# Kernel optimization log

Measured on AMD Instinct MI355X. Metric: run time of the kernel, lower is better.

The kernel has to match this reference:

```python
import jax, jax.numpy as jnp
import numpy as np

N = 100000
E = 1600000
U_DIM = 8
H_DIM = 64
MLP_H = 32
LRELU_SLOPE = 0.01  # torch LeakyReLU default


def _linear_params(key, fan_in, fan_out):
    # torch nn.Linear init: U(-1/sqrt(fan_in), 1/sqrt(fan_in))
    k1, k2 = jax.random.split(key)
    bound = 1.0 / np.sqrt(fan_in)
    W = jax.random.uniform(k1, (fan_in, fan_out), minval=-bound, maxval=bound, dtype=jnp.float32)
    b = jax.random.uniform(k2, (fan_out,), minval=-bound, maxval=bound, dtype=jnp.float32)
    return W, b


def setup_inputs() -> dict:
    key = jax.random.key(0)
    ks = jax.random.split(key, 9)
    h = jax.random.normal(ks[0], (N, H_DIM), dtype=jnp.float32)
    u = jax.random.normal(ks[1], (N, U_DIM), dtype=jnp.float32)
    pos = jax.random.normal(ks[2], (N, 2), dtype=jnp.float32)
    src = jax.random.randint(ks[3], (E,), 0, N)
    dst = jax.random.randint(ks[4], (E,), 0, N)
    # edge MLP (u2h_enc): in = 4 + u_dim + h_dim
    W1e, b1e = _linear_params(ks[5], 4 + U_DIM + H_DIM, MLP_H)
    W2e, b2e = _linear_params(ks[6], MLP_H, H_DIM)
    # node MLP (h_updater): in = 2 + 2*h_dim + u_dim
    W1n, b1n = _linear_params(ks[7], 2 + 2 * H_DIM + U_DIM, MLP_H)
    W2n, b2n = _linear_params(ks[8], MLP_H, H_DIM)
    return {"h": h, "u": u, "pos": pos, "src": src, "dst": dst,
            "W1e": W1e, "b1e": b1e, "W2e": W2e, "b2e": b2e,
            "W1n": W1n, "b1n": b1n, "W2n": W2n, "b2n": b2n}


def _mlp(x, W1, b1, W2, b2):
    # Linear -> LeakyReLU -> Linear -> Tanh
    y = x @ W1 + b1
    y = jnp.where(y >= 0, y, LRELU_SLOPE * y)
    return jnp.tanh(y @ W2 + b2)


def reference(h, u, pos, src, dst, W1e, b1e, W2e, b2e, W1n, b1n, W2n, b2n):
    # gather: edge message input [E, 4+u+h]
    edge_inp = jnp.concatenate([pos[src], pos[dst], u[src], h[src]], axis=-1)
    msg = _mlp(edge_inp, W1e, b1e, W2e, b2e)  # [E, h_dim]
    # scatter-sum into destination nodes
    sum_h = jax.ops.segment_sum(msg, dst, num_segments=N)  # [N, h_dim]
    node_inp = jnp.concatenate([pos, h, sum_h, u], axis=-1)  # [N, 2+2h+u]
    return _mlp(node_inp, W1n, b1n, W2n, b2n)
```

## Files before the change

kernel.cpp:

```cpp
#include <hip/hip_runtime.h>


#define LRELU_SLOPE 0.01f
#define BUCK_SHIFT 8
#define TANH_SCALE 2.8853900817779268f

constexpr int OFF_B1E   = 2432;
constexpr int OFF_B2E   = 4512;
constexpr int OFF_B2N   = 11104;
constexpr int OFF_B1N   = 11168;
constexpr int OFF_W1POS = 11200;
constexpr int W_TOTAL   = 11264;

typedef __bf16 bf16x8 __attribute__((ext_vector_type(8)));
typedef float  f32x4  __attribute__((ext_vector_type(4)));

__device__ __forceinline__ unsigned f2bf_pair(float f0, float f1) {
    unsigned u0 = __float_as_uint(f0), u1 = __float_as_uint(f1);
    unsigned r0 = (u0 + 0x7fffu + ((u0 >> 16) & 1u)) >> 16;
    unsigned r1 = (u1 + 0x7fffu + ((u1 >> 16) & 1u)) >> 16;
    return r0 | (r1 << 16);
}
__device__ __forceinline__ float bf_lo(unsigned p) { return __uint_as_float(p << 16); }
__device__ __forceinline__ float bf_hi(unsigned p) { return __uint_as_float(p & 0xffff0000u); }
__device__ __forceinline__ float bf_round(float f) {
    unsigned u = __float_as_uint(f);
    return __uint_as_float((u + 0x7fffu + ((u >> 16) & 1u)) & 0xffff0000u);
}
__device__ __forceinline__ bf16x8 pack8(float a0, float a1, float a2, float a3,
                                        float a4, float a5, float a6, float a7) {
    union { uint4 u; bf16x8 b; } c;
    c.u.x = f2bf_pair(a0, a1); c.u.y = f2bf_pair(a2, a3);
    c.u.z = f2bf_pair(a4, a5); c.u.w = f2bf_pair(a6, a7);
    return c.b;
}

__device__ __forceinline__ float w1e_x96(const float* W1e, int i, int j) {
    if (i < 64) return W1e[(12 + i) * 32 + j];
    if (i == 64) return W1e[0 * 32 + j];
    if (i == 65) return W1e[1 * 32 + j];
    if (i >= 68 && i < 76) return W1e[(4 + i - 68) * 32 + j];
    return 0.f;
}
__device__ __forceinline__ float w1n_x96(const float* W1n, int i, int j) {
    if (i < 64) return W1n[(2 + i) * 32 + j];
    if (i == 64) return W1n[0 * 32 + j];
    if (i == 65) return W1n[1 * 32 + j];
    if (i >= 68 && i < 76) return W1n[(130 + i - 68) * 32 + j];
    return 0.f;
}

__global__ void prep_weights(const float* __restrict__ W1e, const float* __restrict__ b1e,
                             const float* __restrict__ W2e, const float* __restrict__ b2e,
                             const float* __restrict__ W1n, const float* __restrict__ b1n,
                             const float* __restrict__ W2n, const float* __restrict__ b2n,
                             float* __restrict__ Wf, uint4* __restrict__ fragW2,
                             uint4* __restrict__ frag1, uint4* __restrict__ frag2,
                             uint4* __restrict__ fragE, uint4* __restrict__ fragN,
                             int* __restrict__ gcnt, int nbuck) {
    int t = blockIdx.x * blockDim.x + threadIdx.x;
    int T = gridDim.x * blockDim.x;
    for (int idx = t; idx < nbuck; idx += T) gcnt[idx] = 0;
    for (int idx = t; idx < 32; idx += T)   Wf[OFF_B1E + idx] = b1e[idx];
    for (int idx = t; idx < 64; idx += T)   Wf[OFF_B2E + idx] = b2e[idx] * TANH_SCALE;
    for (int idx = t; idx < 64; idx += T)   Wf[OFF_B2N + idx] = b2n[idx];
    for (int idx = t; idx < 32; idx += T)   Wf[OFF_B1N + idx] = b1n[idx];
    for (int idx = t; idx < 32; idx += T) {
        Wf[OFF_W1POS + 2 * idx + 0] = W1e[2 * 32 + idx];
        Wf[OFF_W1POS + 2 * idx + 1] = W1e[3 * 32 + idx];
    }
    for (int idx = t; idx < 256; idx += T) {
        int tt = idx >> 6, l = idx & 63;
        int colv = l & 15, quadv = l >> 4;
        uint4 v;
        unsigned pk[4];
#pragma unroll
        for (int pr = 0; pr < 4; pr++) {
            int j0 = quadv * 8 + 2 * pr;
            float f0 = W2e[j0 * 64 + 16 * tt + colv] * TANH_SCALE;
            float f1 = W2e[(j0 + 1) * 64 + 16 * tt + colv] * TANH_SCALE;
            pk[pr] = f2bf_pair(f0, f1);
        }
        v.x = pk[0]; v.y = pk[1]; v.z = pk[2]; v.w = pk[3];
        fragW2[tt * 64 + l] = v;
    }
    for (int idx = t; idx < 512; idx += T) {
        int l = idx & 63, rest = idx >> 6;
        int hl = rest & 1, tt = (rest >> 1) & 1, kc = rest >> 2;
        int colv = l & 15, quadv = l >> 4;
        unsigned pk[4];
#pragma unroll
        for (int pr = 0; pr < 4; pr++) {
            int i0 = kc * 32 + quadv * 8 + 2 * pr;
            float f0 = W1n[(66 + i0) * 32 + tt * 16 + colv];
            float f1 = W1n[(66 + i0 + 1) * 32 + tt * 16 + colv];
            if (hl) { f0 -= bf_round(f0); f1 -= bf_round(f1); }
            pk[pr] = f2bf_pair(f0, f1);
        }
        uint4 v; v.x = pk[0]; v.y = pk[1]; v.z = pk[2]; v.w = pk[3];
        frag1[idx] = v;
    }
    for (int idx = t; idx < 512; idx += T) {
        int l = idx & 63, rest = idx >> 6;
        int hl = rest & 1, tt = rest >> 1;
        int colv = l & 15, quadv = l >> 4;
        unsigned pk[4];
#pragma unroll
        for (int pr = 0; pr < 4; pr++) {
            int j0 = quadv * 8 + 2 * pr;
            float f0 = W2n[j0 * 64 + tt * 16 + colv] * TANH_SCALE;
            float f1 = W2n[(j0 + 1) * 64 + tt * 16 + colv] * TANH_SCALE;
            if (hl) { f0 -= bf_round(f0); f1 -= bf_round(f1); }
            pk[pr] = f2bf_pair(f0, f1);
        }
        uint4 v; v.x = pk[0]; v.y = pk[1]; v.z = pk[2]; v.w = pk[3];
        frag2[idx] = v;
    }
    for (int idx = t; idx < 768; idx += T) {
        int l = idx & 63, rest = idx >> 6;
        int hl = rest & 1, tt = (rest >> 1) & 1, kc = rest >> 2;
        int colv = l & 15, quadv = l >> 4;
        int j = tt * 16 + colv;
        unsigned pkE[4], pkN[4];
#pragma unroll
        for (int pr = 0; pr < 4; pr++) {
            int i0 = kc * 32 + quadv * 8 + 2 * pr;
            float e0 = w1e_x96(W1e, i0, j), e1 = w1e_x96(W1e, i0 + 1, j);
            float n0 = w1n_x96(W1n, i0, j), n1 = w1n_x96(W1n, i0 + 1, j);
            if (hl) {
                e0 -= bf_round(e0); e1 -= bf_round(e1);
                n0 -= bf_round(n0); n1 -= bf_round(n1);
            }
            pkE[pr] = f2bf_pair(e0, e1);
            pkN[pr] = f2bf_pair(n0, n1);
        }
        uint4 ve; ve.x = pkE[0]; ve.y = pkE[1]; ve.z = pkE[2]; ve.w = pkE[3];
        uint4 vn; vn.x = pkN[0]; vn.y = pkN[1]; vn.z = pkN[2]; vn.w = pkN[3];
        fragE[idx] = ve;
        fragN[idx] = vn;
    }
}

__global__ __launch_bounds__(256) void k_phase1(
    const float* __restrict__ hbuf, const float* __restrict__ ubuf,
    const float* __restrict__ posbuf, const float* __restrict__ Wf,
    const uint4* __restrict__ fragE, const uint4* __restrict__ fragN,
    uint4* __restrict__ Abf, float* __restrict__ A2,
    const int* __restrict__ src, const int* __restrict__ dst,
    int* __restrict__ gcnt, unsigned* __restrict__ pairbuf,
    int E, int N, int C, int nblkA) {
    __shared__ int cnt[512], base[512];
    __shared__ float tileE[4 * 16 * 36], tileN[4 * 16 * 36];
    int tid = threadIdx.x;
    if ((int)blockIdx.x < nblkA) {
        for (int i = tid; i < 512; i += 256) cnt[i] = 0;
        __syncthreads();
        int e0 = blockIdx.x * 2048;
#pragma unroll
        for (int k = 0; k < 8; k++) {
            int e = e0 + k * 256 + tid;
            if (e < E) atomicAdd(&cnt[dst[e] >> BUCK_SHIFT], 1);
        }
        __syncthreads();
        for (int i = tid; i < 512; i += 256) {
            int c = cnt[i];
            base[i] = (c > 0) ? atomicAdd(&gcnt[i], c) : 0;
            cnt[i] = 0;
        }
        __syncthreads();
#pragma unroll
        for (int k = 0; k < 8; k++) {
            int e = e0 + k * 256 + tid;
            if (e < E) {
                int d = dst[e];
                int b = d >> BUCK_SHIFT;
                int r = base[b] + atomicAdd(&cnt[b], 1);
                if (r < C)
                    pairbuf[(size_t)b * C + r] =
                        (unsigned)src[e] | ((unsigned)(d & 255) << 20);
            }
        }
        return;
    }
    int wv = tid >> 6, lane = tid & 63;
    int col = lane & 15, quad = lane >> 4;
    int g = ((int)blockIdx.x - nblkA) * 4 + wv;
    int ngroups = (N + 15) >> 4;
    if (g >= ngroups) return;
    int nbase = g * 16;
    int nA = nbase + col; nA = (nA < N) ? nA : (N - 1);

    bf16x8 xh[3], xl[3];
    {
        const float* hrow = hbuf + (size_t)nA * 64 + quad * 8;
        float4 f0 = *(const float4*)(hrow);
        float4 f1 = *(const float4*)(hrow + 4);
        xh[0] = pack8(f0.x, f0.y, f0.z, f0.w, f1.x, f1.y, f1.z, f1.w);
        xl[0] = pack8(f0.x - bf_round(f0.x), f0.y - bf_round(f0.y),
                      f0.z - bf_round(f0.z), f0.w - bf_round(f0.w),
                      f1.x - bf_round(f1.x), f1.y - bf_round(f1.y),
                      f1.z - bf_round(f1.z), f1.w - bf_round(f1.w));
        float4 g0 = *(const float4*)(hrow + 32);
        float4 g1 = *(const float4*)(hrow + 36);
        xh[1] = pack8(g0.x, g0.y, g0.z, g0.w, g1.x, g1.y, g1.z, g1.w);
        xl[1] = pack8(g0.x - bf_round(g0.x), g0.y - bf_round(g0.y),
                      g0.z - bf_round(g0.z), g0.w - bf_round(g0.w),
                      g1.x - bf_round(g1.x), g1.y - bf_round(g1.y),
                      g1.z - bf_round(g1.z), g1.w - bf_round(g1.w));
    }
    {
        float xv[8];
#pragma unroll
        for (int i = 0; i < 8; i++) xv[i] = 0.f;
        if (quad == 0) {
            float2 pp = ((const float2*)posbuf)[nA];
            float4 uu = ((const float4*)ubuf)[(size_t)nA * 2];
            xv[0] = pp.x; xv[1] = pp.y;
            xv[4] = uu.x; xv[5] = uu.y; xv[6] = uu.z; xv[7] = uu.w;
        } else if (quad == 1) {
            float4 ub = ((const float4*)ubuf)[(size_t)nA * 2 + 1];
            xv[0] = ub.x; xv[1] = ub.y; xv[2] = ub.z; xv[3] = ub.w;
        }
        xh[2] = pack8(xv[0], xv[1], xv[2], xv[3], xv[4], xv[5], xv[6], xv[7]);
        xl[2] = pack8(xv[0] - bf_round(xv[0]), xv[1] - bf_round(xv[1]),
                      xv[2] - bf_round(xv[2]), xv[3] - bf_round(xv[3]),
                      xv[4] - bf_round(xv[4]), xv[5] - bf_round(xv[5]),
                      xv[6] - bf_round(xv[6]), xv[7] - bf_round(xv[7]));
    }

    f32x4 accE[2], accN[2];
#pragma unroll
    for (int t = 0; t < 2; t++) {
        float be = Wf[OFF_B1E + t * 16 + col];
        float bn = Wf[OFF_B1N + t * 16 + col];
        f32x4 e = {be, be, be, be}; accE[t] = e;
        f32x4 n = {bn, bn, bn, bn}; accN[t] = n;
    }
#pragma unroll
    for (int kc = 0; kc < 3; kc++) {
#pragma unroll
        for (int t = 0; t < 2; t++) {
            union { uint4 u; bf16x8 b; } bh, bl;
            int fi = ((kc * 2 + t) * 2) * 64 + lane;
            bh.u = fragE[fi]; bl.u = fragE[fi + 64];
            accE[t] = __builtin_amdgcn_mfma_f32_16x16x32_bf16(xh[kc], bh.b, accE[t], 0, 0, 0);
            accE[t] = __builtin_amdgcn_mfma_f32_16x16x32_bf16(xh[kc], bl.b, accE[t], 0, 0, 0);
            accE[t] = __builtin_amdgcn_mfma_f32_16x16x32_bf16(xl[kc], bh.b, accE[t], 0, 0, 0);
            bh.u = fragN[fi]; bl.u = fragN[fi + 64];
            accN[t] = __builtin_amdgcn_mfma_f32_16x16x32_bf16(xh[kc], bh.b, accN[t], 0, 0, 0);
            accN[t] = __builtin_amdgcn_mfma_f32_16x16x32_bf16(xh[kc], bl.b, accN[t], 0, 0, 0);
            accN[t] = __builtin_amdgcn_mfma_f32_16x16x32_bf16(xl[kc], bh.b, accN[t], 0, 0, 0);
        }
    }

    float* twE = tileE + wv * 576;
    float* twN = tileN + wv * 576;
#pragma unroll
    for (int t = 0; t < 2; t++) {
#pragma unroll
        for (int r = 0; r < 4; r++) {
            twE[(quad * 4 + r) * 36 + t * 16 + col] = accE[t][r];
            twN[(quad * 4 + r) * 36 + t * 16 + col] = accN[t][r];
        }
    }
    {
        int node = lane >> 2, q = lane & 3;
        const float* tr = twE + node * 36 + q * 8;
        uint4 v;
        v.x = f2bf_pair(tr[0], tr[1]); v.y = f2bf_pair(tr[2], tr[3]);
        v.z = f2bf_pair(tr[4], tr[5]); v.w = f2bf_pair(tr[6], tr[7]);
        if (nbase + node < N) Abf[(size_t)(nbase + node) * 4 + q] = v;
    }
#pragma unroll
    for (int it = 0; it < 2; it++) {
        int fi = lane + it * 64;
        int node = fi >> 3, c = fi & 7;
        float4 fv = *(const float4*)(twN + node * 36 + c * 4);
        if (nbase + node < N)
            ((float4*)(A2 + (size_t)(nbase + node) * 32))[c] = fv;
    }
}

extern __shared__ unsigned pls[];
__global__ __launch_bounds__(512) void k_bucketB(
    const unsigned* __restrict__ pairbuf, const int* __restrict__ gcnt,
    int2* __restrict__ seg, int* __restrict__ ssrc, int N, int C) {
    __shared__ int deg[256], scn[256], exc[256], cur[256];
    int b = blockIdx.x, tid = threadIdx.x;
    int cntb = gcnt[b];
    cntb = (cntb < C) ? cntb : C;
    if (tid < 256) { deg[tid] = 0; cur[tid] = 0; }
    __syncthreads();
    size_t basep = (size_t)b * C;
    for (int i = tid; i < cntb; i += 512)
        atomicAdd(&deg[pairbuf[basep + i] >> 20], 1);
    __syncthreads();
    if (tid < 256) scn[tid] = deg[tid];
    __syncthreads();
    for (int st = 1; st < 256; st <<= 1) {
        int add = (tid < 256 && tid >= st) ? scn[tid - st] : 0;
        __syncthreads();
        if (tid < 256) scn[tid] += add;
        __syncthreads();
    }
    if (tid < 256) {
        int ex = scn[tid] - deg[tid];
        exc[tid] = ex;
        int n = (b << BUCK_SHIFT) + tid;
        if (n < N) {
            int lo = b * C + ex;
            seg[n] = make_int2(lo, lo + deg[tid]);
        }
    }
    __syncthreads();
    for (int i = tid; i < cntb; i += 512) {
        unsigned p = pairbuf[basep + i];
        int l = (int)(p >> 20);
        int slot = exc[l] + atomicAdd(&cur[l], 1);
        pls[slot] = p & 0xFFFFFu;
    }
    __syncthreads();
    for (int i = tid; i < cntb; i += 512)
        ssrc[basep + i] = (int)pls[i];
}

__global__ __launch_bounds__(256) void fused_edge_gather(
    const int2* __restrict__ seg, const int* __restrict__ ssrc,
    const uint4* __restrict__ Abf, const float* __restrict__ posbuf,
    const float* __restrict__ Wf, const uint4* __restrict__ fragW2,
    float* __restrict__ sumh, int N, int npw) {
    int wid = blockIdx.x * 4 + (threadIdx.x >> 6);
    int lane = threadIdx.x & 63;
    int col = lane & 15, quad = lane >> 4;

    union { uint4 u; bf16x8 v; } cvt;
    bf16x8 bfr[4];
#pragma unroll
    for (int t = 0; t < 4; t++) {
        cvt.u = fragW2[t * 64 + lane];
        bfr[t] = cvt.v;
    }
    float c0[4];
#pragma unroll
    for (int t = 0; t < 4; t++) c0[t] = Wf[OFF_B2E + 16 * t + col];
    float wx[8], wy[8];
#pragma unroll
    for (int jj = 0; jj < 8; jj++) {
        float2 wv = ((const float2*)(Wf + OFF_W1POS))[quad * 8 + jj];
        wx[jj] = wv.x; wy[jj] = wv.y;
    }

    int n0 = wid * npw;
    int n1 = n0 + npw; n1 = (n1 < N) ? n1 : N;
#pragma unroll 1
    for (int n = n0; n < n1; n++) {
        int2 sg = seg[n];
        int lo = sg.x, hi = sg.y, deg = hi - lo;
        float2 pd = ((const float2*)posbuf)[n];
        float padd[8];
#pragma unroll
        for (int jj = 0; jj < 8; jj++)
            padd[jj] = fmaf(pd.x, wx[jj], pd.y * wy[jj]);

        float s0[4] = {0.f, 0.f, 0.f, 0.f};
        if (deg > 0) {
            int te = lo + col;
            te = (te < hi) ? te : (hi - 1);
            uint4 ar = Abf[(size_t)ssrc[te] * 4 + quad];
            int nfull = deg & ~15;
#pragma unroll 1
            for (int b = 0; b < nfull; b += 16) {
                int teN = lo + b + 16 + col;
                teN = (teN < hi) ? teN : (hi - 1);
                uint4 arN = Abf[(size_t)ssrc[teN] * 4 + quad];

                bf16x8 af;
                {
                    float v0 = bf_lo(ar.x) + padd[0], v1 = bf_hi(ar.x) + padd[1];
                    float v2 = bf_lo(ar.y) + padd[2], v3 = bf_hi(ar.y) + padd[3];
                    float v4 = bf_lo(ar.z) + padd[4], v5 = bf_hi(ar.z) + padd[5];
                    float v6 = bf_lo(ar.w) + padd[6], v7 = bf_hi(ar.w) + padd[7];
                    v0 = fmaxf(v0, LRELU_SLOPE * v0); v1 = fmaxf(v1, LRELU_SLOPE * v1);
                    v2 = fmaxf(v2, LRELU_SLOPE * v2); v3 = fmaxf(v3, LRELU_SLOPE * v3);
                    v4 = fmaxf(v4, LRELU_SLOPE * v4); v5 = fmaxf(v5, LRELU_SLOPE * v5);
                    v6 = fmaxf(v6, LRELU_SLOPE * v6); v7 = fmaxf(v7, LRELU_SLOPE * v7);
                    af[0] = (__bf16)v0; af[1] = (__bf16)v1; af[2] = (__bf16)v2; af[3] = (__bf16)v3;
                    af[4] = (__bf16)v4; af[5] = (__bf16)v5; af[6] = (__bf16)v6; af[7] = (__bf16)v7;
                }
#pragma unroll
                for (int t = 0; t < 4; t++) {
                    f32x4 acc = {c0[t], c0[t], c0[t], c0[t]};
                    acc = __builtin_amdgcn_mfma_f32_16x16x32_bf16(af, bfr[t], acc, 0, 0, 0);
                    float u0 = __builtin_amdgcn_exp2f(acc[0]);
                    float u1 = __builtin_amdgcn_exp2f(acc[1]);
                    float u2 = __builtin_amdgcn_exp2f(acc[2]);
                    float u3 = __builtin_amdgcn_exp2f(acc[3]);
                    float q01 = u0 + u1, q23 = u2 + u3;
                    float d01 = fmaf(u0, u1, q01) + 1.f;
                    float d23 = fmaf(u2, u3, q23) + 1.f;
                    s0[t] = fmaf(q01 + 2.f, __builtin_amdgcn_rcpf(d01), s0[t]);
                    s0[t] = fmaf(q23 + 2.f, __builtin_amdgcn_rcpf(d23), s0[t]);
                }
                ar = arN;
            }
            int tail = deg - nfull;
            if (tail) {
                bf16x8 af;
                {
                    float v0 = bf_lo(ar.x) + padd[0], v1 = bf_hi(ar.x) + padd[1];
                    float v2 = bf_lo(ar.y) + padd[2], v3 = bf_hi(ar.y) + padd[3];
                    float v4 = bf_lo(ar.z) + padd[4], v5 = bf_hi(ar.z) + padd[5];
                    float v6 = bf_lo(ar.w) + padd[6], v7 = bf_hi(ar.w) + padd[7];
                    v0 = fmaxf(v0, LRELU_SLOPE * v0); v1 = fmaxf(v1, LRELU_SLOPE * v1);
                    v2 = fmaxf(v2, LRELU_SLOPE * v2); v3 = fmaxf(v3, LRELU_SLOPE * v3);
                    v4 = fmaxf(v4, LRELU_SLOPE * v4); v5 = fmaxf(v5, LRELU_SLOPE * v5);
                    v6 = fmaxf(v6, LRELU_SLOPE * v6); v7 = fmaxf(v7, LRELU_SLOPE * v7);
                    af[0] = (__bf16)v0; af[1] = (__bf16)v1; af[2] = (__bf16)v2; af[3] = (__bf16)v3;
                    af[4] = (__bf16)v4; af[5] = (__bf16)v5; af[6] = (__bf16)v6; af[7] = (__bf16)v7;
                }
                int rowb = quad * 4;
#pragma unroll
                for (int t = 0; t < 4; t++) {
                    f32x4 acc = {c0[t], c0[t], c0[t], c0[t]};
                    acc = __builtin_amdgcn_mfma_f32_16x16x32_bf16(af, bfr[t], acc, 0, 0, 0);
                    float u0 = (rowb + 0 < tail) ? __builtin_amdgcn_exp2f(acc[0]) : 1e30f;
                    float u1 = (rowb + 1 < tail) ? __builtin_amdgcn_exp2f(acc[1]) : 1e30f;
                    float u2 = (rowb + 2 < tail) ? __builtin_amdgcn_exp2f(acc[2]) : 1e30f;
                    float u3 = (rowb + 3 < tail) ? __builtin_amdgcn_exp2f(acc[3]) : 1e30f;
                    float q01 = u0 + u1, q23 = u2 + u3;
                    float d01 = fmaf(u0, u1, q01) + 1.f;
                    float d23 = fmaf(u2, u3, q23) + 1.f;
                    s0[t] = fmaf(q01 + 2.f, __builtin_amdgcn_rcpf(d01), s0[t]);
                    s0[t] = fmaf(q23 + 2.f, __builtin_amdgcn_rcpf(d23), s0[t]);
                }
            }
        }
#pragma unroll
        for (int t = 0; t < 4; t++) {
            s0[t] += __shfl_xor(s0[t], 16);
            s0[t] += __shfl_xor(s0[t], 32);
        }
        if (lane < 16) {
            float* sr = sumh + (size_t)n * 64;
            float fd = (float)deg;
#pragma unroll
            for (int t = 0; t < 4; t++) sr[16 * t + lane] = fmaf(-2.f, s0[t], fd);
        }
    }
}

__global__ __launch_bounds__(256) void k_node4(
    const float* __restrict__ A2, const float* __restrict__ sumh,
    const float* __restrict__ Wf, const uint4* __restrict__ frag1,
    const uint4* __restrict__ frag2, float* __restrict__ out,
    int N, int ngroups) {
    __shared__ float ylds[4 * 16 * 36];
    int wv = threadIdx.x >> 6, lane = threadIdx.x & 63;
    int col = lane & 15, quad = lane >> 4;
    int g = blockIdx.x * 4 + wv;
    bool live = (g < ngroups);
    int gc = live ? g : (ngroups - 1);
    int nbase = gc * 16;

    int nA = nbase + col; nA = (nA < N) ? nA : (N - 1);
    const float* srow = sumh + (size_t)nA * 64 + quad * 8;
    bf16x8 sh[2], sl[2];
#pragma unroll
    for (int kc = 0; kc < 2; kc++) {
        float4 f0 = *(const float4*)(srow + kc * 32);
        float4 f1 = *(const float4*)(srow + kc * 32 + 4);
        sh[kc] = pack8(f0.x, f0.y, f0.z, f0.w, f1.x, f1.y, f1.z, f1.w);
        sl[kc] = pack8(f0.x - bf_round(f0.x), f0.y - bf_round(f0.y),
                       f0.z - bf_round(f0.z), f0.w - bf_round(f0.w),
                       f1.x - bf_round(f1.x), f1.y - bf_round(f1.y),
                       f1.z - bf_round(f1.z), f1.w - bf_round(f1.w));
    }

    f32x4 acc1[2];
#pragma unroll
    for (int t = 0; t < 2; t++) { f32x4 z = {0.f, 0.f, 0.f, 0.f}; acc1[t] = z; }
#pragma unroll
    for (int kc = 0; kc < 2; kc++) {
#pragma unroll
        for (int t = 0; t < 2; t++) {
            union { uint4 u; bf16x8 b; } bh, bl;
            bh.u = frag1[((kc * 2 + t) * 2 + 0) * 64 + lane];
            bl.u = frag1[((kc * 2 + t) * 2 + 1) * 64 + lane];
            acc1[t] = __builtin_amdgcn_mfma_f32_16x16x32_bf16(sh[kc], bh.b, acc1[t], 0, 0, 0);
            acc1[t] = __builtin_amdgcn_mfma_f32_16x16x32_bf16(sh[kc], bl.b, acc1[t], 0, 0, 0);
            acc1[t] = __builtin_amdgcn_mfma_f32_16x16x32_bf16(sl[kc], bh.b, acc1[t], 0, 0, 0);
        }
    }

    float* yw = ylds + wv * 576;
#pragma unroll
    for (int t = 0; t < 2; t++) {
#pragma unroll
        for (int r = 0; r < 4; r++) {
            int ndr = quad * 4 + r;
            int nd = nbase + ndr; nd = (nd < N) ? nd : (N - 1);
            float yv = acc1[t][r] + A2[(size_t)nd * 32 + t * 16 + col];
            yv = fmaxf(yv, LRELU_SLOPE * yv);
            yw[ndr * 36 + t * 16 + col] = yv;
        }
    }
    __syncthreads();

    const float* yr = ylds + wv * 576 + col * 36 + quad * 8;
    float4 y0 = *(const float4*)(yr);
    float4 y1 = *(const float4*)(yr + 4);
    bf16x8 yh = pack8(y0.x, y0.y, y0.z, y0.w, y1.x, y1.y, y1.z, y1.w);
    bf16x8 yl = pack8(y0.x - bf_round(y0.x), y0.y - bf_round(y0.y),
                      y0.z - bf_round(y0.z), y0.w - bf_round(y0.w),
                      y1.x - bf_round(y1.x), y1.y - bf_round(y1.y),
                      y1.z - bf_round(y1.z), y1.w - bf_round(y1.w));

    f32x4 acc2[4];
#pragma unroll
    for (int t = 0; t < 4; t++) {
        float b = Wf[OFF_B2N + t * 16 + col] * TANH_SCALE;
        f32x4 z = {b, b, b, b}; acc2[t] = z;
    }
#pragma unroll
    for (int t = 0; t < 4; t++) {
        union { uint4 u; bf16x8 b; } bh, bl;
        bh.u = frag2[(t * 2 + 0) * 64 + lane];
        bl.u = frag2[(t * 2 + 1) * 64 + lane];
        acc2[t] = __builtin_amdgcn_mfma_f32_16x16x32_bf16(yh, bh.b, acc2[t], 0, 0, 0);
        acc2[t] = __builtin_amdgcn_mfma_f32_16x16x32_bf16(yh, bl.b, acc2[t], 0, 0, 0);
        acc2[t] = __builtin_amdgcn_mfma_f32_16x16x32_bf16(yl, bh.b, acc2[t], 0, 0, 0);
    }
    if (live) {
#pragma unroll
        for (int t = 0; t < 4; t++) {
#pragma unroll
            for (int r = 0; r < 4; r++) {
                int nd = nbase + quad * 4 + r;
                if (nd < N) {
                    float e = __builtin_amdgcn_exp2f(acc2[t][r]);
                    out[(size_t)nd * 64 + t * 16 + col] =
                        1.f - 2.f * __builtin_amdgcn_rcpf(e + 1.f);
                }
            }
        }
    }
}

extern "C" void kernel_launch(void* const* d_in, const int* in_sizes, int n_in,
                              void* d_out, int out_size, void* d_ws, size_t ws_size,
                              hipStream_t stream) {
    const float* hbuf   = (const float*)d_in[0];
    const float* ubuf   = (const float*)d_in[1];
    const float* posbuf = (const float*)d_in[2];
    const int* src = (const int*)d_in[3];
    const int* dst = (const int*)d_in[4];

    int N = in_sizes[0] / 64;
    int E = in_sizes[3];
    int NBUCK = (N + 255) >> BUCK_SHIFT;
    int C = ((2 * ((E + NBUCK - 1) / NBUCK)) + 255) & ~255;
    int nblkA = (E + 2047) / 2048;

    char* p = (char*)d_ws;
    auto alloc = [&](size_t bytes) {
        char* r = p;
        p += (bytes + 255) & ~(size_t)255;
        return r;
    };
    float*    Wf      = (float*)alloc(W_TOTAL * 4);
    uint4*    fragW2  = (uint4*)alloc(4 * 64 * 16);
    uint4*    frag1   = (uint4*)alloc(512 * 16);
    uint4*    frag2   = (uint4*)alloc(512 * 16);
    uint4*    fragE   = (uint4*)alloc(768 * 16);
    uint4*    fragN   = (uint4*)alloc(768 * 16);
    uint4*    Abf     = (uint4*)alloc((size_t)N * 64);
    float*    A2      = (float*)alloc((size_t)N * 32 * 4);
    float*    sumh    = (float*)alloc((size_t)N * 64 * 4);
    int2*     seg     = (int2*)alloc((size_t)N * 8);
    int*      gcnt    = (int*)alloc((size_t)NBUCK * 4);
    unsigned* pairbuf = (unsigned*)alloc((size_t)NBUCK * C * 4);
    int*      ssrc    = (int*)alloc((size_t)NBUCK * C * 4);

    prep_weights<<<32, 256, 0, stream>>>(
        (const float*)d_in[5], (const float*)d_in[6],
        (const float*)d_in[7], (const float*)d_in[8],
        (const float*)d_in[9], (const float*)d_in[10],
        (const float*)d_in[11], (const float*)d_in[12], Wf, fragW2,
        frag1, frag2, fragE, fragN, gcnt, NBUCK);

    int ngroups = (N + 15) / 16;
    int nblkP = nblkA + (ngroups + 3) / 4;
    k_phase1<<<nblkP, 256, 0, stream>>>(
        hbuf, ubuf, posbuf, Wf, fragE, fragN, Abf, A2, src, dst,
        gcnt, pairbuf, E, N, C, nblkA);

    k_bucketB<<<NBUCK, 512, (size_t)C * 4, stream>>>(
        pairbuf, gcnt, seg, ssrc, N, C);

    const int FBLK = 2048;
    int npw = (N + FBLK * 4 - 1) / (FBLK * 4);
    fused_edge_gather<<<FBLK, 256, 0, stream>>>(
        seg, ssrc, Abf, posbuf, Wf, fragW2, sumh, N, npw);

    k_node4<<<(ngroups + 3) / 4, 256, 0, stream>>>(
        A2, sumh, Wf, frag1, frag2, (float*)d_out, N, ngroups);
}
```

Before: 235.4 us.

## Replace atomic bucket scatter with block-local sort and gather-based bucketing

The edge bucketing step changes. Before, each block did global atomics into bucket counters and made scattered writes into per-bucket slots. Now each 4096-edge block sorts its edges by bucket in shared memory and writes them out contiguously, along with a per-bucket offset/count table. The bucket kernel then prefix-scans those counts and gathers its runs. This removes the global atomics and the gcnt zeroing, but splits the node-precompute kernel off from the bucketing so they no longer overlap in one launch. It also adds a serial per-thread run copy and scatters ssrc writes directly to global memory instead of staging them in shared memory.

After: 224.8 us. 4.5% less time.

```diff
diff --git a/kernel.cpp b/kernel.cpp
--- a/kernel.cpp
+++ b/kernel.cpp
@@ -4,6 +4,7 @@
 #define LRELU_SLOPE 0.01f
 #define BUCK_SHIFT 8
 #define TANH_SCALE 2.8853900817779268f
+#define EPB 4096
 
 constexpr int OFF_B1E   = 2432;
 constexpr int OFF_B2E   = 4512;
@@ -56,11 +57,9 @@
                              const float* __restrict__ W2n, const float* __restrict__ b2n,
                              float* __restrict__ Wf, uint4* __restrict__ fragW2,
                              uint4* __restrict__ frag1, uint4* __restrict__ frag2,
-                             uint4* __restrict__ fragE, uint4* __restrict__ fragN,
-                             int* __restrict__ gcnt, int nbuck) {
+                             uint4* __restrict__ fragE, uint4* __restrict__ fragN) {
     int t = blockIdx.x * blockDim.x + threadIdx.x;
     int T = gridDim.x * blockDim.x;
-    for (int idx = t; idx < nbuck; idx += T) gcnt[idx] = 0;
     for (int idx = t; idx < 32; idx += T)   Wf[OFF_B1E + idx] = b1e[idx];
     for (int idx = t; idx < 64; idx += T)   Wf[OFF_B2E + idx] = b2e[idx] * TANH_SCALE;
     for (int idx = t; idx < 64; idx += T)   Wf[OFF_B2N + idx] = b2n[idx];
@@ -141,50 +140,16 @@
     }
 }
 
-__global__ __launch_bounds__(256) void k_phase1(
+__global__ __launch_bounds__(256) void k_pre(
     const float* __restrict__ hbuf, const float* __restrict__ ubuf,
     const float* __restrict__ posbuf, const float* __restrict__ Wf,
     const uint4* __restrict__ fragE, const uint4* __restrict__ fragN,
-    uint4* __restrict__ Abf, float* __restrict__ A2,
-    const int* __restrict__ src, const int* __restrict__ dst,
-    int* __restrict__ gcnt, unsigned* __restrict__ pairbuf,
-    int E, int N, int C, int nblkA) {
-    __shared__ int cnt[512], base[512];
+    uint4* __restrict__ Abf, float* __restrict__ A2, int N) {
     __shared__ float tileE[4 * 16 * 36], tileN[4 * 16 * 36];
     int tid = threadIdx.x;
-    if ((int)blockIdx.x < nblkA) {
-        for (int i = tid; i < 512; i += 256) cnt[i] = 0;
-        __syncthreads();
-        int e0 = blockIdx.x * 2048;
-#pragma unroll
-        for (int k = 0; k < 8; k++) {
-            int e = e0 + k * 256 + tid;
-            if (e < E) atomicAdd(&cnt[dst[e] >> BUCK_SHIFT], 1);
-        }
-        __syncthreads();
-        for (int i = tid; i < 512; i += 256) {
-            int c = cnt[i];
-            base[i] = (c > 0) ? atomicAdd(&gcnt[i], c) : 0;
-            cnt[i] = 0;
-        }
-        __syncthreads();
-#pragma unroll
-        for (int k = 0; k < 8; k++) {
-            int e = e0 + k * 256 + tid;
-            if (e < E) {
-                int d = dst[e];
-                int b = d >> BUCK_SHIFT;
-                int r = base[b] + atomicAdd(&cnt[b], 1);
-                if (r < C)
-                    pairbuf[(size_t)b * C + r] =
-                        (unsigned)src[e] | ((unsigned)(d & 255) << 20);
-            }
-        }
-        return;
-    }
     int wv = tid >> 6, lane = tid & 63;
     int col = lane & 15, quad = lane >> 4;
-    int g = ((int)blockIdx.x - nblkA) * 4 + wv;
+    int g = (int)blockIdx.x * 4 + wv;
     int ngroups = (N + 15) >> 4;
     if (g >= ngroups) return;
     int nbase = g * 16;
@@ -263,6 +228,7 @@
             twN[(quad * 4 + r) * 36 + t * 16 + col] = accN[t][r];
         }
     }
+    __syncthreads();
     {
         int node = lane >> 2, q = lane & 3;
         const float* tr = twE + node * 36 + q * 8;
@@ -281,19 +247,87 @@
     }
 }
 
-extern __shared__ unsigned pls[];
-__global__ __launch_bounds__(512) void k_bucketB(
-    const unsigned* __restrict__ pairbuf, const int* __restrict__ gcnt,
-    int2* __restrict__ seg, int* __restrict__ ssrc, int N, int C) {
+__global__ __launch_bounds__(512) void k_sortA(
+    const int* __restrict__ src, const int* __restrict__ dst,
+    unsigned* __restrict__ blockbuf, unsigned* __restrict__ packoff, int E) {
+    __shared__ int cnt[512], scn[512], exc[512], cur[512];
+    __shared__ unsigned sorted[EPB];
+    int k = blockIdx.x, tid = threadIdx.x;
+    int e0 = k * EPB;
+    cnt[tid] = 0; cur[tid] = 0;
+    __syncthreads();
+    int bs[8]; unsigned pv[8];
+#pragma unroll
+    for (int j = 0; j < 8; j++) {
+        int e = e0 + j * 512 + tid;
+        if (e < E) {
+            int d = dst[e];
+            bs[j] = d >> BUCK_SHIFT;
+            pv[j] = (unsigned)src[e] | ((unsigned)(d & 255) << 20);
+            atomicAdd(&cnt[bs[j]], 1);
+        } else bs[j] = -1;
+    }
+    __syncthreads();
+    scn[tid] = cnt[tid];
+    __syncthreads();
+    for (int st = 1; st < 512; st <<= 1) {
+        int add = (tid >= st) ? scn[tid - st] : 0;
+        __syncthreads();
+        scn[tid] += add;
+        __syncthreads();
+    }
+    int ex = scn[tid] - cnt[tid];
+    exc[tid] = ex;
+    packoff[(size_t)tid * 512 + k] = ((unsigned)ex << 13) | (unsigned)cnt[tid];
+    __syncthreads();
+    int tot = scn[511];
+#pragma unroll
+    for (int j = 0; j < 8; j++) {
+        if (bs[j] >= 0) {
+            int slot = exc[bs[j]] + atomicAdd(&cur[bs[j]], 1);
+            sorted[slot] = pv[j];
+        }
+    }
+    __syncthreads();
+#pragma unroll
+    for (int j = 0; j < 8; j++) {
+        int i = j * 512 + tid;
+        if (i < tot) blockbuf[(size_t)k * EPB + i] = sorted[i];
+    }
+}
+
+extern __shared__ unsigned gath[];
+__global__ __launch_bounds__(512) void k_bucketB2(
+    const unsigned* __restrict__ blockbuf, const unsigned* __restrict__ packoff,
+    int2* __restrict__ seg, int* __restrict__ ssrc, int N, int C, int nsort) {
+    __shared__ int runc[512];
     __shared__ int deg[256], scn[256], exc[256], cur[256];
     int b = blockIdx.x, tid = threadIdx.x;
-    int cntb = gcnt[b];
+    unsigned po = packoff[(size_t)b * 512 + tid];
+    int rcnt = (tid < nsort) ? (int)(po & 0x1FFFu) : 0;
+    int rexc = (int)(po >> 13);
+    runc[tid] = rcnt;
+    __syncthreads();
+    for (int st = 1; st < 512; st <<= 1) {
+        int add = (tid >= st) ? runc[tid - st] : 0;
+        __syncthreads();
+        runc[tid] += add;
+        __syncthreads();
+    }
+    int my0 = runc[tid] - rcnt;
+    int cntb = runc[511];
     cntb = (cntb < C) ? cntb : C;
+    if (tid < nsort && rcnt > 0) {
+        const unsigned* rb = blockbuf + (size_t)tid * EPB + rexc;
+        for (int i = 0; i < rcnt; i++) {
+            int o = my0 + i;
+            if (o < C) gath[o] = rb[i];
+        }
+    }
     if (tid < 256) { deg[tid] = 0; cur[tid] = 0; }
     __syncthreads();
-    size_t basep = (size_t)b * C;
     for (int i = tid; i < cntb; i += 512)
-        atomicAdd(&deg[pairbuf[basep + i] >> 20], 1);
+        atomicAdd(&deg[gath[i] >> 20], 1);
     __syncthreads();
     if (tid < 256) scn[tid] = deg[tid];
     __syncthreads();
@@ -304,24 +338,22 @@
         __syncthreads();
     }
     if (tid < 256) {
-        int ex = scn[tid] - deg[tid];
-        exc[tid] = ex;
+        int ex2 = scn[tid] - deg[tid];
+        exc[tid] = ex2;
         int n = (b << BUCK_SHIFT) + tid;
         if (n < N) {
-            int lo = b * C + ex;
+            int lo = b * C + ex2;
             seg[n] = make_int2(lo, lo + deg[tid]);
         }
     }
     __syncthreads();
+    size_t basep = (size_t)b * C;
     for (int i = tid; i < cntb; i += 512) {
-        unsigned p = pairbuf[basep + i];
+        unsigned p = gath[i];
         int l = (int)(p >> 20);
         int slot = exc[l] + atomicAdd(&cur[l], 1);
-        pls[slot] = p & 0xFFFFFu;
-    }
-    __syncthreads();
-    for (int i = tid; i < cntb; i += 512)
-        ssrc[basep + i] = (int)pls[i];
+        ssrc[basep + slot] = (int)(p & 0xFFFFFu);
+    }
 }
 
 __global__ __launch_bounds__(256) void fused_edge_gather(
@@ -559,7 +591,7 @@
     int E = in_sizes[3];
     int NBUCK = (N + 255) >> BUCK_SHIFT;
     int C = ((2 * ((E + NBUCK - 1) / NBUCK)) + 255) & ~255;
-    int nblkA = (E + 2047) / 2048;
+    int NSORT = (E + EPB - 1) / EPB;
 
     char* p = (char*)d_ws;
     auto alloc = [&](size_t bytes) {
@@ -567,35 +599,35 @@
         p += (bytes + 255) & ~(size_t)255;
         return r;
     };
-    float*    Wf      = (float*)alloc(W_TOTAL * 4);
-    uint4*    fragW2  = (uint4*)alloc(4 * 64 * 16);
-    uint4*    frag1   = (uint4*)alloc(512 * 16);
-    uint4*    frag2   = (uint4*)alloc(512 * 16);
-    uint4*    fragE   = (uint4*)alloc(768 * 16);
-    uint4*    fragN   = (uint4*)alloc(768 * 16);
-    uint4*    Abf     = (uint4*)alloc((size_t)N * 64);
-    float*    A2      = (float*)alloc((size_t)N * 32 * 4);
-    float*    sumh    = (float*)alloc((size_t)N * 64 * 4);
-    int2*     seg     = (int2*)alloc((size_t)N * 8);
-    int*      gcnt    = (int*)alloc((size_t)NBUCK * 4);
-    unsigned* pairbuf = (unsigned*)alloc((size_t)NBUCK * C * 4);
-    int*      ssrc    = (int*)alloc((size_t)NBUCK * C * 4);
+    float*    Wf       = (float*)alloc(W_TOTAL * 4);
+    uint4*    fragW2   = (uint4*)alloc(4 * 64 * 16);
+    uint4*    frag1    = (uint4*)alloc(512 * 16);
+    uint4*    frag2    = (uint4*)alloc(512 * 16);
+    uint4*    fragE    = (uint4*)alloc(768 * 16);
+    uint4*    fragN    = (uint4*)alloc(768 * 16);
+    uint4*    Abf      = (uint4*)alloc((size_t)N * 64);
+    float*    A2       = (float*)alloc((size_t)N * 32 * 4);
+    float*    sumh     = (float*)alloc((size_t)N * 64 * 4);
+    int2*     seg      = (int2*)alloc((size_t)N * 8);
+    unsigned* blockbuf = (unsigned*)alloc((size_t)NSORT * EPB * 4);
+    unsigned* packoff  = (unsigned*)alloc((size_t)512 * 512 * 4);
+    int*      ssrc     = (int*)alloc((size_t)NBUCK * C * 4);
 
     prep_weights<<<32, 256, 0, stream>>>(
         (const float*)d_in[5], (const float*)d_in[6],
         (const float*)d_in[7], (const float*)d_in[8],
         (const float*)d_in[9], (const float*)d_in[10],
         (const float*)d_in[11], (const float*)d_in[12], Wf, fragW2,
-        frag1, frag2, fragE, fragN, gcnt, NBUCK);
+        frag1, frag2, fragE, fragN);
 
     int ngroups = (N + 15) / 16;
-    int nblkP = nblkA + (ngroups + 3) / 4;
-    k_phase1<<<nblkP, 256, 0, stream>>>(
-        hbuf, ubuf, posbuf, Wf, fragE, fragN, Abf, A2, src, dst,
-        gcnt, pairbuf, E, N, C, nblkA);
-
-    k_bucketB<<<NBUCK, 512, (size_t)C * 4, stream>>>(
-        pairbuf, gcnt, seg, ssrc, N, C);
+    k_pre<<<(ngroups + 3) / 4, 256, 0, stream>>>(
+        hbuf, ubuf, posbuf, Wf, fragE, fragN, Abf, A2, N);
+
+    k_sortA<<<NSORT, 512, 0, stream>>>(src, dst, blockbuf, packoff, E);
+
+    k_bucketB2<<<NBUCK, 512, (size_t)C * 4, stream>>>(
+        blockbuf, packoff, seg, ssrc, N, C, NSORT);
 
     const int FBLK = 2048;
     int npw = (N + FBLK * 4 - 1) / (FBLK * 4);
```
